# Performance work log

Hardware: AMD Instinct MI355X
Metric: run time of the kernel (lower is better)

## Reference

```python
import jax, jax.numpy as jnp
import numpy as np

# Module hyperparameters (from init_kwargs), reduced LJ units
CUTOFF = 2.5
EPSILON = 1.0
SIGMA = 1.0
# Energy shift so the potential is zero at the cutoff, exactly as in __init__
SHIFT = 4.0 * EPSILON * ((SIGMA / CUTOFF) ** 12 - (SIGMA / CUTOFF) ** 6)

N_ATOMS = 262144
AVG_NEIGHBORS = 32
N_PAIRS = N_ATOMS * AVG_NEIGHBORS


def setup_inputs() -> dict:
    key = jax.random.key(0)
    k1, k2, k3 = jax.random.split(key, 3)
    # Half neighbor list: [P, 2] (first_atom, second_atom)
    pairs = jax.random.randint(k1, (N_PAIRS, 2), 0, N_ATOMS, dtype=jnp.int32)
    # Displacement vectors with |r| in [0.9, cutoff] so LJ energies are well-behaved
    r = jax.random.uniform(k2, (N_PAIRS,), minval=0.9, maxval=CUTOFF, dtype=jnp.float32)
    dirs = jax.random.normal(k3, (N_PAIRS, 3), dtype=jnp.float32)
    dirs = dirs / jnp.linalg.norm(dirs, axis=1, keepdims=True)
    distances = dirs * r[:, None]
    return {"pairs": pairs, "distances": distances, "n_atoms": N_ATOMS}


def reference(pairs, distances, n_atoms):
    # Per-pair Lennard-Jones energy: 4*eps*((sigma/r)^12 - (sigma/r)^6) - shift
    r2 = jnp.sum(distances * distances, axis=1)          # [P]
    sr2 = (SIGMA * SIGMA) / r2
    sr6 = sr2 * sr2 * sr2
    e_pair = 4.0 * EPSILON * (sr6 * sr6 - sr6) - SHIFT    # [P]
    # Half list: each pair contributes half its energy to each of its atoms
    half = 0.5 * e_pair
    energy = jax.ops.segment_sum(half, pairs[:, 0], num_segments=n_atoms)
    energy = energy + jax.ops.segment_sum(half, pairs[:, 1], num_segments=n_atoms)
    # TensorBlock values: per-atom energies as a [n_atoms, 1] column
    return energy.reshape(-1, 1)
```

## Files before the change

### kernel.cpp

```cpp
#include <hip/hip_runtime.h>
#include <hip/hip_fp16.h>

__device__ __forceinline__ float half_lj(float r2) {
    float sr2 = 1.0f / r2;
    float sr6 = sr2 * sr2 * sr2;
    return fmaf(2.0f, sr6 * sr6 - sr6, 0.0081584448f);
}

#define SL_SHIFT 14
#define SL_SZ    16384
#define NS_MAX   16
#define NB       256
#define BCAP     48

__device__ __forceinline__ unsigned pack_rec(int atom, float e) {
    unsigned h = (unsigned)__half_as_ushort(__float2half(e));
    return (h << 16) | ((unsigned)atom & (SL_SZ - 1));
}

__global__ __launch_bounds__(256)
void bin_kernel(const int4* __restrict__ pairs4, const float4* __restrict__ dist4,
                unsigned* __restrict__ grec, unsigned* __restrict__ gcnt,
                int npair4, int bucket_cap) {
    __shared__ unsigned staged[NB * BCAP];
    __shared__ unsigned cnt[NB];
    __shared__ unsigned gbase[NB];
    const int tid = threadIdx.x;
    cnt[tid] = 0;
    __syncthreads();

#define STAGE(atom, ev)                                                        \
    do {                                                                       \
        int _a = (atom);                                                       \
        int _b = (unsigned)_a >> 10;                                           \
        unsigned _r = pack_rec(_a, (ev));                                      \
        unsigned _pos = atomicAdd(&cnt[_b], 1u);                               \
        if (_pos < BCAP) {                                                     \
            staged[_b * BCAP + _pos] = _r;                                     \
        } else {                                                               \
            unsigned _gi = atomicAdd(&gcnt[_b], 1u);                           \
            if (_gi < (unsigned)bucket_cap)                                    \
                grec[(size_t)_b * bucket_cap + _gi] = _r;                      \
        }                                                                      \
    } while (0)

    for (int k = 0; k < 4; ++k) {
        int q = (blockIdx.x << 10) + (k << 8) + tid;
        if (q < npair4) {
            int4 pA = pairs4[2 * q];
            int4 pB = pairs4[2 * q + 1];
            float4 d0 = dist4[3 * q], d1 = dist4[3 * q + 1], d2 = dist4[3 * q + 2];
            float e0 = half_lj(fmaf(d0.x, d0.x, fmaf(d0.y, d0.y, d0.z * d0.z)));
            float e1 = half_lj(fmaf(d0.w, d0.w, fmaf(d1.x, d1.x, d1.y * d1.y)));
            float e2 = half_lj(fmaf(d1.z, d1.z, fmaf(d1.w, d1.w, d2.x * d2.x)));
            float e3 = half_lj(fmaf(d2.y, d2.y, fmaf(d2.z, d2.z, d2.w * d2.w)));
            STAGE(pA.x, e0); STAGE(pA.y, e0);
            STAGE(pA.z, e1); STAGE(pA.w, e1);
            STAGE(pB.x, e2); STAGE(pB.y, e2);
            STAGE(pB.z, e3); STAGE(pB.w, e3);
        }
    }
#undef STAGE
    __syncthreads();

    {
        unsigned c = cnt[tid] < BCAP ? cnt[tid] : BCAP;
        gbase[tid] = atomicAdd(&gcnt[tid], c);
    }
    __syncthreads();

    for (int idx = tid; idx < NB * BCAP; idx += 256) {
        int b = idx / BCAP;
        int i = idx - b * BCAP;
        unsigned c = cnt[b] < BCAP ? cnt[b] : BCAP;
        if ((unsigned)i < c) {
            unsigned pos = gbase[b] + i;
            if (pos < (unsigned)bucket_cap)
                grec[(size_t)b * bucket_cap + pos] = staged[idx];
        }
    }
}

__global__ void bin_tail_kernel(const int* __restrict__ pairs,
                                const float* __restrict__ dist,
                                unsigned* __restrict__ grec,
                                unsigned* __restrict__ gcnt,
                                int start, int npairs, int bucket_cap) {
    int i = start + blockIdx.x * 64 + threadIdx.x;
    if (i >= npairs) return;
    float dx = dist[3 * i], dy = dist[3 * i + 1], dz = dist[3 * i + 2];
    float h = half_lj(fmaf(dx, dx, fmaf(dy, dy, dz * dz)));
    int a0 = pairs[2 * i], a1 = pairs[2 * i + 1];
    int b0 = (unsigned)a0 >> 10, b1 = (unsigned)a1 >> 10;
    unsigned g0 = atomicAdd(&gcnt[b0], 1u);
    if (g0 < (unsigned)bucket_cap) grec[(size_t)b0 * bucket_cap + g0] = pack_rec(a0, h);
    unsigned g1 = atomicAdd(&gcnt[b1], 1u);
    if (g1 < (unsigned)bucket_cap) grec[(size_t)b1 * bucket_cap + g1] = pack_rec(a1, h);
}

__global__ __launch_bounds__(1024)
void accum_tag_kernel(const unsigned* __restrict__ grec,
                      const unsigned* __restrict__ gcnt,
                      float* __restrict__ rep,
                      int bucket_cap, int CH, int n_pad) {
    __shared__ float acc[SL_SZ];
    __shared__ unsigned char tag[SL_SZ];
    volatile unsigned char* vtag = tag;
    const int s = blockIdx.x / CH;
    const int c = blockIdx.x % CH;
    const int tid = threadIdx.x;
    const int wave = tid >> 6;
    const int lane = tid & 63;

    float4* acc4 = (float4*)acc;
    for (int i = tid; i < SL_SZ / 4; i += 1024)
        acc4[i] = make_float4(0.f, 0.f, 0.f, 0.f);
    __syncthreads();

    const int b = (s << 4) | wave;
    int M = (int)gcnt[b];
    if (M > bucket_cap) M = bucket_cap;
    const unsigned* base = grec + (size_t)b * bucket_cap;
    const int beg = (int)((long long)c * M / CH);
    const int end = (int)((long long)(c + 1) * M / CH);

    for (int jj = beg; jj < end; jj += 64) {
        int j = jj + lane;
        bool valid = j < end;
        unsigned rec = valid ? base[j] : 0u;
        int a = rec & (SL_SZ - 1);
        float v = __half2float(__ushort_as_half((unsigned short)(rec >> 16)));
        bool active = valid;
        while (__any(active)) {
            if (active) vtag[a] = (unsigned char)lane;
            if (active && vtag[a] == (unsigned char)lane) {
                acc[a] += v;
                active = false;
            }
        }
    }
    __syncthreads();

    float4* rep4 = (float4*)(rep + (size_t)c * n_pad + (size_t)s * SL_SZ);
    for (int i = tid; i < SL_SZ / 4; i += 1024)
        rep4[i] = acc4[i];
}

__global__ void reduce_reps_kernel(const float* __restrict__ rep,
                                   float* __restrict__ out,
                                   int n_atoms, int n_pad, int B) {
    int i4 = blockIdx.x * blockDim.x + threadIdx.x;
    int n4 = n_atoms / 4;
    if (i4 < n4) {
        float4 sum = make_float4(0.f, 0.f, 0.f, 0.f);
        for (int b = 0; b < B; ++b) {
            float4 v = *(const float4*)(rep + (size_t)b * n_pad + 4 * (size_t)i4);
            sum.x += v.x; sum.y += v.y; sum.z += v.z; sum.w += v.w;
        }
        ((float4*)out)[i4] = sum;
    }
    if (i4 == 0) {
        for (int i = n4 * 4; i < n_atoms; ++i) {
            float sum = 0.f;
            for (int b = 0; b < B; ++b) sum += rep[(size_t)b * n_pad + i];
            out[i] = sum;
        }
    }
}

#define PB_SHIFT 15
#define PB_SZ 32768

__global__ void compute_e8_kernel(const float4* __restrict__ dist4,
                                  uint4* __restrict__ e8, int npair8) {
    int t = blockIdx.x * blockDim.x + threadIdx.x;
    if (t >= npair8) return;
    float4 v0 = dist4[6 * t + 0], v1 = dist4[6 * t + 1], v2 = dist4[6 * t + 2];
    float4 v3 = dist4[6 * t + 3], v4 = dist4[6 * t + 4], v5 = dist4[6 * t + 5];
    float h0 = half_lj(fmaf(v0.x, v0.x, fmaf(v0.y, v0.y, v0.z * v0.z)));
    float h1 = half_lj(fmaf(v0.w, v0.w, fmaf(v1.x, v1.x, v1.y * v1.y)));
    float h2 = half_lj(fmaf(v1.z, v1.z, fmaf(v1.w, v1.w, v2.x * v2.x)));
    float h3 = half_lj(fmaf(v2.y, v2.y, fmaf(v2.z, v2.z, v2.w * v2.w)));
    float h4 = half_lj(fmaf(v3.x, v3.x, fmaf(v3.y, v3.y, v3.z * v3.z)));
    float h5 = half_lj(fmaf(v3.w, v3.w, fmaf(v4.x, v4.x, v4.y * v4.y)));
    float h6 = half_lj(fmaf(v4.z, v4.z, fmaf(v4.w, v4.w, v5.x * v5.x)));
    float h7 = half_lj(fmaf(v5.y, v5.y, fmaf(v5.z, v5.z, v5.w * v5.w)));
    union { __half2 h; unsigned u; } c01, c23, c45, c67;
    c01.h = __floats2half2_rn(h0, h1);
    c23.h = __floats2half2_rn(h2, h3);
    c45.h = __floats2half2_rn(h4, h5);
    c67.h = __floats2half2_rn(h6, h7);
    uint4 o; o.x = c01.u; o.y = c23.u; o.z = c45.u; o.w = c67.u;
    e8[t] = o;
}

__global__ void compute_e_tail_kernel(const float* __restrict__ dist,
                                      __half* __restrict__ eh,
                                      int start, int npairs) {
    int i = start + blockIdx.x * blockDim.x + threadIdx.x;
    if (i >= npairs) return;
    float dx = dist[3 * i], dy = dist[3 * i + 1], dz = dist[3 * i + 2];
    eh[i] = __float2half(half_lj(fmaf(dx, dx, fmaf(dy, dy, dz * dz))));
}

__global__ __launch_bounds__(1024, 1)
void accum_slice_kernel(const int4* __restrict__ pairs4,
                        const uint2* __restrict__ eh2,
                        const int* __restrict__ pairs,
                        const __half* __restrict__ eh,
                        float* __restrict__ rep,
                        int npair4, int npairs, int nslices, int B, int n_pad) {
    __shared__ float lds[PB_SZ];
    int gid = blockIdx.x;
    int s = gid % nslices;
    int b = gid / nslices;
    const int tid = threadIdx.x;
    const int base = s << PB_SHIFT;

    float4* lds4 = (float4*)lds;
    for (int i = tid; i < PB_SZ / 4; i += 1024)
        lds4[i] = make_float4(0.f, 0.f, 0.f, 0.f);
    __syncthreads();

    const int qb = (int)((long long)b * npair4 / B);
    const int qe = (int)((long long)(b + 1) * npair4 / B);

#define CHK(atom, val)                                           \
    do {                                                         \
        int _t = (atom) - base;                                  \
        if ((unsigned)_t < PB_SZ) atomicAdd(&lds[_t], (val));    \
    } while (0)

    for (int q = qb + tid; q < qe; q += 1024) {
        int4 pA = pairs4[2 * q];
        int4 pB = pairs4[2 * q + 1];
        uint2 ue = eh2[q];
        union { unsigned u; __half2 h; } a_, b_;
        a_.u = ue.x; b_.u = ue.y;
        float2 e01 = __half22float2(a_.h);
        float2 e23 = __half22float2(b_.h);
        CHK(pA.x, e01.x); CHK(pA.y, e01.x);
        CHK(pA.z, e01.y); CHK(pA.w, e01.y);
        CHK(pB.x, e23.x); CHK(pB.y, e23.x);
        CHK(pB.z, e23.y); CHK(pB.w, e23.y);
    }
    if (b == 0) {
        for (int i = npair4 * 4 + tid; i < npairs; i += 1024) {
            int a0 = pairs[2 * i], a1 = pairs[2 * i + 1];
            float h = __half2float(eh[i]);
            CHK(a0, h);
            CHK(a1, h);
        }
    }
#undef CHK
    __syncthreads();

    float4* rep4 = (float4*)(rep + (size_t)b * n_pad + (size_t)s * PB_SZ);
    for (int i = tid; i < PB_SZ / 4; i += 1024)
        rep4[i] = lds4[i];
}

__global__ void lj_vec4_agent_kernel(const int4* __restrict__ pairs4,
                                     const float4* __restrict__ dist4,
                                     float* __restrict__ out, int npair4) {
    int t = blockIdx.x * blockDim.x + threadIdx.x;
    if (t >= npair4) return;
    int4 p01 = pairs4[2 * t];
    int4 p23 = pairs4[2 * t + 1];
    float4 d0 = dist4[3 * t];
    float4 d1 = dist4[3 * t + 1];
    float4 d2 = dist4[3 * t + 2];
    float h0 = half_lj(fmaf(d0.x, d0.x, fmaf(d0.y, d0.y, d0.z * d0.z)));
    float h1 = half_lj(fmaf(d0.w, d0.w, fmaf(d1.x, d1.x, d1.y * d1.y)));
    float h2 = half_lj(fmaf(d1.z, d1.z, fmaf(d1.w, d1.w, d2.x * d2.x)));
    float h3 = half_lj(fmaf(d2.y, d2.y, fmaf(d2.z, d2.z, d2.w * d2.w)));
    unsafeAtomicAdd(&out[p01.x], h0);
    unsafeAtomicAdd(&out[p01.y], h0);
    unsafeAtomicAdd(&out[p01.z], h1);
    unsafeAtomicAdd(&out[p01.w], h1);
    unsafeAtomicAdd(&out[p23.x], h2);
    unsafeAtomicAdd(&out[p23.y], h2);
    unsafeAtomicAdd(&out[p23.z], h3);
    unsafeAtomicAdd(&out[p23.w], h3);
}

__global__ void lj_tail_agent_kernel(const int* __restrict__ pairs,
                                     const float* __restrict__ dist,
                                     float* __restrict__ out,
                                     int start, int npairs) {
    int i = start + blockIdx.x * blockDim.x + threadIdx.x;
    if (i >= npairs) return;
    float dx = dist[3 * i], dy = dist[3 * i + 1], dz = dist[3 * i + 2];
    float h = half_lj(fmaf(dx, dx, fmaf(dy, dy, dz * dz)));
    unsafeAtomicAdd(&out[pairs[2 * i]], h);
    unsafeAtomicAdd(&out[pairs[2 * i + 1]], h);
}

extern "C" void kernel_launch(void* const* d_in, const int* in_sizes, int n_in,
                              void* d_out, int out_size, void* d_ws, size_t ws_size,
                              hipStream_t stream) {
    const int* pairs = (const int*)d_in[0];
    const float* dist = (const float*)d_in[1];
    float* out = (float*)d_out;

    const int n_atoms = out_size;
    const int npairs = in_sizes[0] / 2;
    const int npair4 = npairs / 4;

    const int nslices = (n_atoms + SL_SZ - 1) >> SL_SHIFT;
    if (n_atoms <= NB * 1024 && nslices <= NS_MAX && npairs > 0) {
        const int n_pad = nslices << SL_SHIFT;
        int bucket_cap = (int)(2LL * npairs / NB + 2048);
        size_t cnt_bytes = 4096;
        size_t rec_bytes = (size_t)NB * (size_t)bucket_cap * 4;
        int CH = 32;
        while (CH > 4 &&
               cnt_bytes + rec_bytes + (size_t)CH * (size_t)n_pad * 4 > ws_size)
            CH >>= 1;
        size_t need = cnt_bytes + rec_bytes + (size_t)CH * (size_t)n_pad * 4;
        if (need <= ws_size) {
            unsigned* gcnt = (unsigned*)d_ws;
            unsigned* grec = (unsigned*)((char*)d_ws + cnt_bytes);
            float* rep = (float*)((char*)d_ws + cnt_bytes + rec_bytes);

            hipMemsetAsync(gcnt, 0, NB * sizeof(unsigned), stream);

            int nb = (npair4 + 1023) / 1024;
            if (nb > 0)
                bin_kernel<<<nb, 256, 0, stream>>>(
                    (const int4*)pairs, (const float4*)dist, grec, gcnt,
                    npair4, bucket_cap);
            if (npair4 * 4 < npairs)
                bin_tail_kernel<<<1, 64, 0, stream>>>(pairs, dist, grec, gcnt,
                                                      npair4 * 4, npairs,
                                                      bucket_cap);

            accum_tag_kernel<<<nslices * CH, 1024, 0, stream>>>(
                grec, gcnt, rep, bucket_cap, CH, n_pad);

            int n4 = n_atoms / 4;
            int grid = (n4 + 255) / 256;
            if (grid == 0) grid = 1;
            reduce_reps_kernel<<<grid, 256, 0, stream>>>(rep, out, n_atoms,
                                                         n_pad, CH);
            return;
        }
    }

    {
        const int nsl = (n_atoms + PB_SZ - 1) >> PB_SHIFT;
        const int n_pad = nsl << PB_SHIFT;
        const size_t e_elems = (size_t)((npairs + 7) / 8) * 8;
        const size_t e_bytes = e_elems * sizeof(__half);
        int B = 32;
        while (B > 8 && e_bytes + (size_t)B * n_pad * sizeof(float) > ws_size)
            B >>= 1;
        if (e_bytes + (size_t)B * n_pad * sizeof(float) <= ws_size) {
            __half* eh = (__half*)d_ws;
            float* rep = (float*)((char*)d_ws + e_bytes);
            int npair8 = npairs / 8;
            if (npair8 > 0)
                compute_e8_kernel<<<(npair8 + 255) / 256, 256, 0, stream>>>(
                    (const float4*)dist, (uint4*)eh, npair8);
            if (npair8 * 8 < npairs)
                compute_e_tail_kernel<<<1, 64, 0, stream>>>(dist, eh,
                                                            npair8 * 8, npairs);
            accum_slice_kernel<<<nsl * B, 1024, 0, stream>>>(
                (const int4*)pairs, (const uint2*)eh, pairs, eh, rep,
                npair4, npairs, nsl, B, n_pad);
            int n4 = n_atoms / 4;
            int grid = (n4 + 255) / 256;
            if (grid == 0) grid = 1;
            reduce_reps_kernel<<<grid, 256, 0, stream>>>(rep, out, n_atoms,
                                                         n_pad, B);
            return;
        }
    }

    hipMemsetAsync(d_out, 0, (size_t)out_size * sizeof(float), stream);
    if (npair4 > 0)
        lj_vec4_agent_kernel<<<(npair4 + 255) / 256, 256, 0, stream>>>(
            (const int4*)pairs, (const float4*)dist, out, npair4);
    if (npair4 * 4 < npairs)
        lj_tail_agent_kernel<<<1, 64, 0, stream>>>(pairs, dist, out,
                                                   npair4 * 4, npairs);
}
```

Before: 128.8 us.

## Replace LDS atomic binning with per-wave tag-based staging and padded global counters

The binning kernel no longer uses shared-memory atomicAdd on a per-block bucket counter. Each wave now keeps its own staging area, and lanes resolve bucket conflicts with a tag/vote loop, in the same style the accumulation kernel already uses. Global bucket counters are also spaced out by 32 words so that atomics on different buckets fall on different cache lines. The change trades LDS atomic contention for serialization retries, a smaller per-wave capacity that spills to global atomics more often, and a larger memset.

```diff
diff --git a/kernel.cpp b/kernel.cpp
--- a/kernel.cpp
+++ b/kernel.cpp
@@ -11,7 +11,8 @@
 #define SL_SZ    16384
 #define NS_MAX   16
 #define NB       256
-#define BCAP     48
+#define WCAP     16
+#define GC_STRIDE 32
 
 __device__ __forceinline__ unsigned pack_rec(int atom, float e) {
     unsigned h = (unsigned)__half_as_ushort(__float2half(e));
@@ -22,31 +23,25 @@
 void bin_kernel(const int4* __restrict__ pairs4, const float4* __restrict__ dist4,
                 unsigned* __restrict__ grec, unsigned* __restrict__ gcnt,
                 int npair4, int bucket_cap) {
-    __shared__ unsigned staged[NB * BCAP];
-    __shared__ unsigned cnt[NB];
+    __shared__ unsigned staged[4][NB][WCAP];
+    __shared__ unsigned char wcnt[4][NB];
+    __shared__ unsigned char tagm[4][NB];
     __shared__ unsigned gbase[NB];
     const int tid = threadIdx.x;
-    cnt[tid] = 0;
-    __syncthreads();
-
-#define STAGE(atom, ev)                                                        \
-    do {                                                                       \
-        int _a = (atom);                                                       \
-        int _b = (unsigned)_a >> 10;                                           \
-        unsigned _r = pack_rec(_a, (ev));                                      \
-        unsigned _pos = atomicAdd(&cnt[_b], 1u);                               \
-        if (_pos < BCAP) {                                                     \
-            staged[_b * BCAP + _pos] = _r;                                     \
-        } else {                                                               \
-            unsigned _gi = atomicAdd(&gcnt[_b], 1u);                           \
-            if (_gi < (unsigned)bucket_cap)                                    \
-                grec[(size_t)_b * bucket_cap + _gi] = _r;                      \
-        }                                                                      \
-    } while (0)
+    const int wave = tid >> 6, lane = tid & 63;
+    wcnt[0][tid & 255] = 0; wcnt[1][tid & 255] = 0;
+    wcnt[2][tid & 255] = 0; wcnt[3][tid & 255] = 0;
+    __syncthreads();
+
+    volatile unsigned char* vtag = &tagm[wave][0];
+    unsigned char* mycnt = &wcnt[wave][0];
 
     for (int k = 0; k < 4; ++k) {
         int q = (blockIdx.x << 10) + (k << 8) + tid;
-        if (q < npair4) {
+        bool valid = q < npair4;
+        unsigned recs[8];
+        int bks[8];
+        if (valid) {
             int4 pA = pairs4[2 * q];
             int4 pB = pairs4[2 * q + 1];
             float4 d0 = dist4[3 * q], d1 = dist4[3 * q + 1], d2 = dist4[3 * q + 2];
@@ -54,29 +49,55 @@
             float e1 = half_lj(fmaf(d0.w, d0.w, fmaf(d1.x, d1.x, d1.y * d1.y)));
             float e2 = half_lj(fmaf(d1.z, d1.z, fmaf(d1.w, d1.w, d2.x * d2.x)));
             float e3 = half_lj(fmaf(d2.y, d2.y, fmaf(d2.z, d2.z, d2.w * d2.w)));
-            STAGE(pA.x, e0); STAGE(pA.y, e0);
-            STAGE(pA.z, e1); STAGE(pA.w, e1);
-            STAGE(pB.x, e2); STAGE(pB.y, e2);
-            STAGE(pB.z, e3); STAGE(pB.w, e3);
-        }
-    }
-#undef STAGE
+            recs[0] = pack_rec(pA.x, e0); bks[0] = (unsigned)pA.x >> 10;
+            recs[1] = pack_rec(pA.y, e0); bks[1] = (unsigned)pA.y >> 10;
+            recs[2] = pack_rec(pA.z, e1); bks[2] = (unsigned)pA.z >> 10;
+            recs[3] = pack_rec(pA.w, e1); bks[3] = (unsigned)pA.w >> 10;
+            recs[4] = pack_rec(pB.x, e2); bks[4] = (unsigned)pB.x >> 10;
+            recs[5] = pack_rec(pB.y, e2); bks[5] = (unsigned)pB.y >> 10;
+            recs[6] = pack_rec(pB.z, e3); bks[6] = (unsigned)pB.z >> 10;
+            recs[7] = pack_rec(pB.w, e3); bks[7] = (unsigned)pB.w >> 10;
+        }
+#pragma unroll
+        for (int r = 0; r < 8; ++r) {
+            bool active = valid;
+            int b = valid ? bks[r] : 0;
+            unsigned rec = valid ? recs[r] : 0u;
+            while (__any(active)) {
+                if (active) vtag[b] = (unsigned char)lane;
+                if (active && vtag[b] == (unsigned char)lane) {
+                    int pos = mycnt[b];
+                    if (pos < WCAP) {
+                        staged[wave][b][pos] = rec;
+                        mycnt[b] = (unsigned char)(pos + 1);
+                    } else {
+                        unsigned gi = atomicAdd(&gcnt[b * GC_STRIDE], 1u);
+                        if (gi < (unsigned)bucket_cap)
+                            grec[(size_t)b * bucket_cap + gi] = rec;
+                    }
+                    active = false;
+                }
+            }
+        }
+    }
     __syncthreads();
 
     {
-        unsigned c = cnt[tid] < BCAP ? cnt[tid] : BCAP;
-        gbase[tid] = atomicAdd(&gcnt[tid], c);
-    }
-    __syncthreads();
-
-    for (int idx = tid; idx < NB * BCAP; idx += 256) {
-        int b = idx / BCAP;
-        int i = idx - b * BCAP;
-        unsigned c = cnt[b] < BCAP ? cnt[b] : BCAP;
-        if ((unsigned)i < c) {
-            unsigned pos = gbase[b] + i;
+        int b = tid;
+        unsigned c = (unsigned)wcnt[0][b] + wcnt[1][b] + wcnt[2][b] + wcnt[3][b];
+        gbase[b] = atomicAdd(&gcnt[b * GC_STRIDE], c);
+    }
+    __syncthreads();
+
+    for (int idx = tid; idx < 4 * NB * WCAP; idx += 256) {
+        int b = idx >> 6;
+        int w = (idx >> 4) & 3;
+        int i = idx & (WCAP - 1);
+        if (i < (int)wcnt[w][b]) {
+            unsigned pos = gbase[b] + (unsigned)i;
+            for (int w2 = 0; w2 < w; ++w2) pos += wcnt[w2][b];
             if (pos < (unsigned)bucket_cap)
-                grec[(size_t)b * bucket_cap + pos] = staged[idx];
+                grec[(size_t)b * bucket_cap + pos] = staged[w][b][i];
         }
     }
 }
@@ -92,9 +113,9 @@
     float h = half_lj(fmaf(dx, dx, fmaf(dy, dy, dz * dz)));
     int a0 = pairs[2 * i], a1 = pairs[2 * i + 1];
     int b0 = (unsigned)a0 >> 10, b1 = (unsigned)a1 >> 10;
-    unsigned g0 = atomicAdd(&gcnt[b0], 1u);
+    unsigned g0 = atomicAdd(&gcnt[b0 * GC_STRIDE], 1u);
     if (g0 < (unsigned)bucket_cap) grec[(size_t)b0 * bucket_cap + g0] = pack_rec(a0, h);
-    unsigned g1 = atomicAdd(&gcnt[b1], 1u);
+    unsigned g1 = atomicAdd(&gcnt[b1 * GC_STRIDE], 1u);
     if (g1 < (unsigned)bucket_cap) grec[(size_t)b1 * bucket_cap + g1] = pack_rec(a1, h);
 }
 
@@ -104,8 +125,8 @@
                       float* __restrict__ rep,
                       int bucket_cap, int CH, int n_pad) {
     __shared__ float acc[SL_SZ];
-    __shared__ unsigned char tag[SL_SZ];
-    volatile unsigned char* vtag = tag;
+    __shared__ unsigned char tagm[SL_SZ];
+    volatile unsigned char* vtag = tagm;
     const int s = blockIdx.x / CH;
     const int c = blockIdx.x % CH;
     const int tid = threadIdx.x;
@@ -118,7 +139,7 @@
     __syncthreads();
 
     const int b = (s << 4) | wave;
-    int M = (int)gcnt[b];
+    int M = (int)gcnt[b * GC_STRIDE];
     if (M > bucket_cap) M = bucket_cap;
     const unsigned* base = grec + (size_t)b * bucket_cap;
     const int beg = (int)((long long)c * M / CH);
@@ -311,7 +332,7 @@
     if (n_atoms <= NB * 1024 && nslices <= NS_MAX && npairs > 0) {
         const int n_pad = nslices << SL_SHIFT;
         int bucket_cap = (int)(2LL * npairs / NB + 2048);
-        size_t cnt_bytes = 4096;
+        size_t cnt_bytes = (size_t)NB * GC_STRIDE * 4;
         size_t rec_bytes = (size_t)NB * (size_t)bucket_cap * 4;
         int CH = 32;
         while (CH > 4 &&
@@ -323,7 +344,7 @@
             unsigned* grec = (unsigned*)((char*)d_ws + cnt_bytes);
             float* rep = (float*)((char*)d_ws + cnt_bytes + rec_bytes);
 
-            hipMemsetAsync(gcnt, 0, NB * sizeof(unsigned), stream);
+            hipMemsetAsync(gcnt, 0, cnt_bytes, stream);
 
             int nb = (npair4 + 1023) / 1024;
             if (nb > 0)
```

New measurement: 232.5 us. 1.8x slower.

## Pad global bucket counters and shrink bin blocks for higher occupancy

Applied to the files above, without the earlier changes.

Spreads each global bucket counter onto its own 128-byte line, so atomics from different buckets no longer contend on shared cache lines. It also halves the pairs handled per bin block and shrinks the LDS staging capacity per bucket, with a launch-bounds hint of 5 blocks per CU, to raise occupancy. The cost is more blocks, each issuing its own per-bucket global atomics, and more overflow records that take the direct global-atomic path because the smaller staging buffer fills sooner.

```diff
diff --git a/kernel.cpp b/kernel.cpp
--- a/kernel.cpp
+++ b/kernel.cpp
@@ -9,19 +9,20 @@
 
 #define SL_SHIFT 14
 #define SL_SZ    16384
-#define NS_MAX   16
 #define NB       256
-#define BCAP     48
+#define BCAP     28
+#define QPB      512
+#define GC_STRIDE 32
 
 __device__ __forceinline__ unsigned pack_rec(int atom, float e) {
     unsigned h = (unsigned)__half_as_ushort(__float2half(e));
     return (h << 16) | ((unsigned)atom & (SL_SZ - 1));
 }
 
-__global__ __launch_bounds__(256)
+__global__ __launch_bounds__(256, 5)
 void bin_kernel(const int4* __restrict__ pairs4, const float4* __restrict__ dist4,
                 unsigned* __restrict__ grec, unsigned* __restrict__ gcnt,
-                int npair4, int bucket_cap) {
+                int npair4, int cap) {
     __shared__ unsigned staged[NB * BCAP];
     __shared__ unsigned cnt[NB];
     __shared__ unsigned gbase[NB];
@@ -37,15 +38,14 @@
         unsigned _pos = atomicAdd(&cnt[_b], 1u);                               \
         if (_pos < BCAP) {                                                     \
             staged[_b * BCAP + _pos] = _r;                                     \
-        } else {                                                               \
-            unsigned _gi = atomicAdd(&gcnt[_b], 1u);                           \
-            if (_gi < (unsigned)bucket_cap)                                    \
-                grec[(size_t)_b * bucket_cap + _gi] = _r;                      \
+        } else {                      \
+            unsigned _gi = atomicAdd(&gcnt[_b * GC_STRIDE], 1u);               \
+            if (_gi < (unsigned)cap) grec[(size_t)_b * cap + _gi] = _r;        \
         }                                                                      \
     } while (0)
 
-    for (int k = 0; k < 4; ++k) {
-        int q = (blockIdx.x << 10) + (k << 8) + tid;
+    for (int k = 0; k < 2; ++k) {
+        int q = blockIdx.x * QPB + (k << 8) + tid;
         if (q < npair4) {
             int4 pA = pairs4[2 * q];
             int4 pB = pairs4[2 * q + 1];
@@ -65,7 +65,7 @@
 
     {
         unsigned c = cnt[tid] < BCAP ? cnt[tid] : BCAP;
-        gbase[tid] = atomicAdd(&gcnt[tid], c);
+        gbase[tid] = atomicAdd(&gcnt[tid * GC_STRIDE], c);
     }
     __syncthreads();
 
@@ -74,9 +74,9 @@
         int i = idx - b * BCAP;
         unsigned c = cnt[b] < BCAP ? cnt[b] : BCAP;
         if ((unsigned)i < c) {
-            unsigned pos = gbase[b] + i;
-            if (pos < (unsigned)bucket_cap)
-                grec[(size_t)b * bucket_cap + pos] = staged[idx];
+            unsigned pos = gbase[b] + (unsigned)i;
+            if (pos < (unsigned)cap)
+                grec[(size_t)b * cap + pos] = staged[idx];
         }
     }
 }
@@ -85,27 +85,27 @@
                                 const float* __restrict__ dist,
                                 unsigned* __restrict__ grec,
                                 unsigned* __restrict__ gcnt,
-                                int start, int npairs, int bucket_cap) {
+                                int start, int npairs, int cap) {
     int i = start + blockIdx.x * 64 + threadIdx.x;
     if (i >= npairs) return;
     float dx = dist[3 * i], dy = dist[3 * i + 1], dz = dist[3 * i + 2];
     float h = half_lj(fmaf(dx, dx, fmaf(dy, dy, dz * dz)));
     int a0 = pairs[2 * i], a1 = pairs[2 * i + 1];
     int b0 = (unsigned)a0 >> 10, b1 = (unsigned)a1 >> 10;
-    unsigned g0 = atomicAdd(&gcnt[b0], 1u);
-    if (g0 < (unsigned)bucket_cap) grec[(size_t)b0 * bucket_cap + g0] = pack_rec(a0, h);
-    unsigned g1 = atomicAdd(&gcnt[b1], 1u);
-    if (g1 < (unsigned)bucket_cap) grec[(size_t)b1 * bucket_cap + g1] = pack_rec(a1, h);
+    unsigned g0 = atomicAdd(&gcnt[b0 * GC_STRIDE], 1u);
+    if (g0 < (unsigned)cap) grec[(size_t)b0 * cap + g0] = pack_rec(a0, h);
+    unsigned g1 = atomicAdd(&gcnt[b1 * GC_STRIDE], 1u);
+    if (g1 < (unsigned)cap) grec[(size_t)b1 * cap + g1] = pack_rec(a1, h);
 }
 
 __global__ __launch_bounds__(1024)
 void accum_tag_kernel(const unsigned* __restrict__ grec,
                       const unsigned* __restrict__ gcnt,
                       float* __restrict__ rep,
-                      int bucket_cap, int CH, int n_pad) {
+                      int cap, int CH, int n_pad) {
     __shared__ float acc[SL_SZ];
-    __shared__ unsigned char tag[SL_SZ];
-    volatile unsigned char* vtag = tag;
+    __shared__ unsigned char tagm[SL_SZ];
+    volatile unsigned char* vtag = tagm;
     const int s = blockIdx.x / CH;
     const int c = blockIdx.x % CH;
     const int tid = threadIdx.x;
@@ -117,10 +117,10 @@
         acc4[i] = make_float4(0.f, 0.f, 0.f, 0.f);
     __syncthreads();
 
-    const int b = (s << 4) | wave;
-    int M = (int)gcnt[b];
-    if (M > bucket_cap) M = bucket_cap;
-    const unsigned* base = grec + (size_t)b * bucket_cap;
+    const int g = (s << 4) | wave;
+    int M = (int)gcnt[g * GC_STRIDE];
+    if (M > cap) M = cap;
+    const unsigned* base = grec + (size_t)g * cap;
     const int beg = (int)((long long)c * M / CH);
     const int end = (int)((long long)(c + 1) * M / CH);
 
@@ -307,12 +307,12 @@
     const int npairs = in_sizes[0] / 2;
     const int npair4 = npairs / 4;
 
-    const int nslices = (n_atoms + SL_SZ - 1) >> SL_SHIFT;
-    if (n_atoms <= NB * 1024 && nslices <= NS_MAX && npairs > 0) {
+    if (n_atoms <= NB * 1024 && npairs > 0) {
+        const int nslices = (n_atoms + SL_SZ - 1) >> SL_SHIFT;
         const int n_pad = nslices << SL_SHIFT;
-        int bucket_cap = (int)(2LL * npairs / NB + 2048);
-        size_t cnt_bytes = 4096;
-        size_t rec_bytes = (size_t)NB * (size_t)bucket_cap * 4;
+        int cap = (int)(2LL * npairs / NB + 2048);
+        size_t cnt_bytes = (size_t)NB * GC_STRIDE * 4;
+        size_t rec_bytes = (size_t)NB * (size_t)cap * 4;
         int CH = 32;
         while (CH > 4 &&
                cnt_bytes + rec_bytes + (size_t)CH * (size_t)n_pad * 4 > ws_size)
@@ -323,20 +323,19 @@
             unsigned* grec = (unsigned*)((char*)d_ws + cnt_bytes);
             float* rep = (float*)((char*)d_ws + cnt_bytes + rec_bytes);
 
-            hipMemsetAsync(gcnt, 0, NB * sizeof(unsigned), stream);
-
-            int nb = (npair4 + 1023) / 1024;
+            hipMemsetAsync(gcnt, 0, cnt_bytes, stream);
+
+            int nb = (npair4 + QPB - 1) / QPB;
             if (nb > 0)
                 bin_kernel<<<nb, 256, 0, stream>>>(
                     (const int4*)pairs, (const float4*)dist, grec, gcnt,
-                    npair4, bucket_cap);
+                    npair4, cap);
             if (npair4 * 4 < npairs)
                 bin_tail_kernel<<<1, 64, 0, stream>>>(pairs, dist, grec, gcnt,
-                                                      npair4 * 4, npairs,
-                                                      bucket_cap);
+                                                      npair4 * 4, npairs, cap);
 
             accum_tag_kernel<<<nslices * CH, 1024, 0, stream>>>(
-                grec, gcnt, rep, bucket_cap, CH, n_pad);
+                grec, gcnt, rep, cap, CH, n_pad);
 
             int n4 = n_atoms / 4;
             int grid = (n4 + 255) / 256;
```

Measured after the change: 130.8 us. Within noise of the previous version (+1.5%).
